# Optimization experiments

Hardware: AMD Instinct MI355X
Metric: run time of the kernel (lower is better)

The kernel has to match this reference:

```python
import jax, jax.numpy as jnp
import numpy as np

N_NODES = 20000
N_EDGES = 320000
L = 512   # input feature dim (size_dict['small'][0])
D = 256   # hidden dim (feat_channel), heads=1 so head_dim = 256
C = 2     # n_classes


def setup_inputs() -> dict:
    key = jax.random.key(0)
    ks = jax.random.split(key, 18)
    s = 0.02
    inp = {
        "x": jax.random.normal(ks[0], (N_NODES, L), jnp.float32),
        "edge_index": jax.random.randint(ks[1], (2, N_EDGES), 0, N_NODES, dtype=jnp.int32),
        "label": 1,
        # TransformerConv(L, D, heads=1): query/key/value + root skip projections
        "Wq": jax.random.normal(ks[2], (L, D), jnp.float32) * s,
        "bq": jax.random.normal(ks[3], (D,), jnp.float32) * s,
        "Wk": jax.random.normal(ks[4], (L, D), jnp.float32) * s,
        "bk": jax.random.normal(ks[5], (D,), jnp.float32) * s,
        "Wv": jax.random.normal(ks[6], (L, D), jnp.float32) * s,
        "bv": jax.random.normal(ks[7], (D,), jnp.float32) * s,
        "Ws": jax.random.normal(ks[8], (L, D), jnp.float32) * s,
        "bs": jax.random.normal(ks[9], (D,), jnp.float32) * s,
        # GlobalAdaptPooling: tanh-MLP attention (heads = n_classes) + per-class classifier
        "Wa1": jax.random.normal(ks[10], (D, D), jnp.float32) * s,
        "ba1": jax.random.normal(ks[11], (D,), jnp.float32) * s,
        "Wa2": jax.random.normal(ks[12], (D, C), jnp.float32) * s,
        "ba2": jax.random.normal(ks[13], (C,), jnp.float32) * s,
        "Wc": jax.random.normal(ks[14], (C, D), jnp.float32) * s,
        "bc": jax.random.normal(ks[15], (C,), jnp.float32) * s,
    }
    return inp


def _forward(x, edge_index, label, Wq, bq, Wk, bk, Wv, bv, Ws, bs, Wa1, ba1, Wa2, ba2, Wc, bc):
    n = x.shape[0]
    src = edge_index[0]  # message source j
    dst = edge_index[1]  # message target i
    # --- TransformerConv (heads=1, concat, root_weight=True) ---
    q = x @ Wq + bq                      # [N, D]
    k = x @ Wk + bk
    v = x @ Wv + bv
    score = jnp.sum(q[dst] * k[src], axis=-1) / jnp.sqrt(jnp.float32(D))  # [E]
    # segment softmax over incoming edges of each target node
    m = jax.ops.segment_max(score, dst, num_segments=n)
    e = jnp.exp(score - m[dst])
    den = jax.ops.segment_sum(e, dst, num_segments=n)
    alpha = e / den[dst]                 # [E]
    agg = jax.ops.segment_sum(alpha[:, None] * v[src], dst, num_segments=n)  # [N, D]
    h = agg + x @ Ws + bs
    # --- act: GELU (torch exact/erf) ---
    h = jax.nn.gelu(h, approximate=False)
    # --- GlobalAdaptPooling: node attention with n_classes heads ---
    scores = jnp.tanh(h @ Wa1 + ba1) @ Wa2 + ba2      # [N, C]
    attn = jax.nn.softmax(scores, axis=0)             # softmax over nodes
    M = attn.T @ h                                    # [C, D] per-class bag embedding
    logits = (jnp.sum(M * Wc, axis=1) + bc)[None, :]  # [1, C]
    Y_prob = jax.nn.softmax(logits, axis=1)
    A = attn[:, label]                                # [N] attention for target class
    return logits, Y_prob, A


def reference(x, edge_index, label, Wq, bq, Wk, bk, Wv, bv, Ws, bs, Wa1, ba1, Wa2, ba2, Wc, bc):
    return _forward(x, edge_index, label, Wq, bq, Wk, bk, Wv, bv, Ws, bs, Wa1, ba1, Wa2, ba2, Wc, bc)
```

## Files before the change

kernel.cpp:

```cpp
#include <hip/hip_runtime.h>
#include <hip/hip_bf16.h>
#include <math.h>

typedef float f32x4_t __attribute__((ext_vector_type(4)));
typedef float f32x2_t __attribute__((ext_vector_type(2)));
typedef __bf16 bf16x8_t __attribute__((ext_vector_type(8)));

__device__ __forceinline__ float bf2f(unsigned int u){
  union { float f; unsigned int i; } x; x.i = u << 16; return x.f;
}
__device__ __forceinline__ unsigned short f2bf(float f){
  unsigned int x = __float_as_uint(f);
  unsigned int r = (x + 0x7fffu + ((x >> 16) & 1u)) >> 16;
  return (unsigned short)r;
}
__device__ __forceinline__ unsigned int pk2bf(float a, float b){
  return (unsigned int)f2bf(a) | ((unsigned int)f2bf(b) << 16);
}
__device__ __forceinline__ int swz4(int r){ return (r ^ (r >> 2) ^ (r >> 4)) & 3; }

__device__ __forceinline__ void unp8s(uint4 w, float* f, float s){
  f[0] = bf2f(w.x & 0xffffu) * s; f[1] = bf2f(w.x >> 16) * s;
  f[2] = bf2f(w.y & 0xffffu) * s; f[3] = bf2f(w.y >> 16) * s;
  f[4] = bf2f(w.z & 0xffffu) * s; f[5] = bf2f(w.z >> 16) * s;
  f[6] = bf2f(w.w & 0xffffu) * s; f[7] = bf2f(w.w >> 16) * s;
}
__device__ __forceinline__ void unpf8(unsigned int w, float* f){
  f32x2_t lo = __builtin_amdgcn_cvt_pk_f32_fp8(w, false);
  f32x2_t hi = __builtin_amdgcn_cvt_pk_f32_fp8(w, true);
  f[0] = lo[0]; f[1] = lo[1]; f[2] = hi[0]; f[3] = hi[1];
}

#define GLOAD16(gsrc, ldst) \
  __builtin_amdgcn_global_load_lds((const __attribute__((address_space(1))) unsigned int*)(gsrc), \
                                   (__attribute__((address_space(3))) unsigned int*)(ldst), 16, 0, 0)

__global__ void zero_buf(uint4* __restrict__ p, int n16){
  int i = blockIdx.x * 256 + threadIdx.x;
  if (i < n16) p[i] = make_uint4(0, 0, 0, 0);
}

__global__ void prep(const float* __restrict__ x,
                     const float* __restrict__ Wq, const float* __restrict__ Wk,
                     const float* __restrict__ Wv, const float* __restrict__ Ws,
                     const float* __restrict__ bq, const float* __restrict__ bk,
                     const float* __restrict__ bv, const float* __restrict__ bs,
                     const float* __restrict__ Wa1, const int* __restrict__ ei,
                     unsigned short* __restrict__ xbf, unsigned short* __restrict__ wcatT,
                     float* __restrict__ bcat, unsigned short* __restrict__ wa1T,
                     int* __restrict__ deg, int n, int ne, int nbcv){
  const int b = blockIdx.x, tid = threadIdx.x;
  if (b < 2048){
    int idx = b * 256 + tid;
    int c = idx >> 9, k = idx & 511;
    int sel = c >> 8, cc = c & 255;
    const float* W = (sel == 0) ? Wq : (sel == 1) ? Wk : (sel == 2) ? Wv : Ws;
    int p = ((k >> 3) & 3) ^ swz4(c & 127);
    int dst = c * 512 + (k & ~31) + p * 8 + (k & 7);
    wcatT[dst] = f2bf(W[k * 256 + cc]);
    if (idx < 1024){
      int sel2 = idx >> 8, cc2 = idx & 255;
      const float* B = (sel2 == 0) ? bq : (sel2 == 1) ? bk : (sel2 == 2) ? bv : bs;
      bcat[idx] = B[cc2];
    }
  } else if (b < 2304){
    int idx = (b - 2048) * 256 + tid;
    int c = idx >> 8, k = idx & 255;
    wa1T[idx] = f2bf(Wa1[k * 256 + c]);
  } else if (b < 2304 + nbcv){
    int idx = (b - 2304) * 256 + tid;
    if (idx < n * 64){
      int node = idx >> 6, un = idx & 63;
      int k0 = (un >> 2) * 32, u = un & 3;
      const float* src = x + (size_t)node * 512 + k0 + u * 8;
      float4 f0 = *reinterpret_cast<const float4*>(src);
      float4 f1 = *reinterpret_cast<const float4*>(src + 4);
      uint4 o;
      o.x = pk2bf(f0.x, f0.y); o.y = pk2bf(f0.z, f0.w);
      o.z = pk2bf(f1.x, f1.y); o.w = pk2bf(f1.z, f1.w);
      int p = u ^ swz4(node & 127);
      *reinterpret_cast<uint4*>(xbf + (size_t)node * 512 + k0 + p * 8) = o;
    }
  } else {
    int i = (b - 2304 - nbcv) * 256 + tid;
    if (i < ne) atomicAdd(&deg[ei[ne + i]], 1);
  }
}

__global__ __launch_bounds__(256) void gemm_qkvs(const unsigned short* __restrict__ xbf,
                                                 const unsigned short* __restrict__ wcatT,
                                                 const float* __restrict__ bcat,
                                                 unsigned short* __restrict__ qbf,
                                                 unsigned short* __restrict__ sbf,
                                                 unsigned char* __restrict__ kv8,
                                                 int n_nodes, int mblocks){
  __shared__ __align__(16) unsigned char smem[49152];
  const int tid = threadIdx.x;
  const int lane = tid & 63, wave = tid >> 6;
  const int wm = wave >> 1, wn = wave & 1;
  const int g = (blockIdx.x & 7) * mblocks + (blockIdx.x >> 3);
  const int m_blk = g >> 3, n_blk = g & 7;
  const int m0 = m_blk * 128, n0 = n_blk * 128;
  const int lrow = lane >> 2;
  const int lcol = (lane & 3) * 8;
  const int rA0 = min(m0 + wave * 16 + lrow, n_nodes - 1);
  const int rA1 = min(m0 + (wave + 4) * 16 + lrow, n_nodes - 1);
  const int rB0 = n0 + wave * 16 + lrow;
  const int rB1 = rB0 + 64;
  const int r = lane & 15, q4 = lane >> 4;
  const unsigned short* aG0 = xbf   + (size_t)rA0 * 512 + lcol;
  const unsigned short* aG1 = xbf   + (size_t)rA1 * 512 + lcol;
  const unsigned short* bG0 = wcatT + (size_t)rB0 * 512 + lcol;
  const unsigned short* bG1 = wcatT + (size_t)rB1 * 512 + lcol;
  int aoff[4], boff[4];
  #pragma unroll
  for (int mi = 0; mi < 4; mi++){ int rr = wm * 64 + mi * 16 + r; aoff[mi] = rr * 32 + ((q4 ^ swz4(rr)) * 8); }
  #pragma unroll
  for (int ni = 0; ni < 4; ni++){ int rb = wn * 64 + ni * 16 + r; boff[ni] = rb * 32 + ((q4 ^ swz4(rb)) * 8); }
  f32x4_t acc[4][4] = {};
#define STAGE(base, k0) { \
    unsigned short* As_ = (unsigned short*)(smem + (base)); \
    unsigned short* Bs_ = (unsigned short*)(smem + (base) + 8192); \
    GLOAD16(aG0 + (k0), &As_[wave * 512]); \
    GLOAD16(aG1 + (k0), &As_[(wave + 4) * 512]); \
    GLOAD16(bG0 + (k0), &Bs_[wave * 512]); \
    GLOAD16(bG1 + (k0), &Bs_[(wave + 4) * 512]); \
  }
  STAGE(0, 0);
  STAGE(16384, 32);
  int cbase = 0;
  int sbase = 32768;
  for (int t = 0; t < 16; t++){
    if (t + 2 < 16){
      STAGE(sbase, (t + 2) * 32);
      asm volatile("s_waitcnt vmcnt(8)" ::: "memory");
    } else if (t + 1 < 16){
      asm volatile("s_waitcnt vmcnt(4)" ::: "memory");
    } else {
      asm volatile("s_waitcnt vmcnt(0)" ::: "memory");
    }
    __builtin_amdgcn_s_barrier();
    asm volatile("" ::: "memory");
    const unsigned short* As = (const unsigned short*)(smem + cbase);
    const unsigned short* Bs = (const unsigned short*)(smem + cbase + 8192);
    bf16x8_t a[4], b[4];
    #pragma unroll
    for (int mi = 0; mi < 4; mi++) a[mi] = *reinterpret_cast<const bf16x8_t*>(&As[aoff[mi]]);
    #pragma unroll
    for (int ni = 0; ni < 4; ni++) b[ni] = *reinterpret_cast<const bf16x8_t*>(&Bs[boff[ni]]);
    #pragma unroll
    for (int mi = 0; mi < 4; mi++)
      #pragma unroll
      for (int ni = 0; ni < 4; ni++)
        acc[mi][ni] = __builtin_amdgcn_mfma_f32_16x16x32_bf16(b[ni], a[mi], acc[mi][ni], 0, 0, 0);
    __builtin_amdgcn_s_barrier();
    asm volatile("" ::: "memory");
    cbase += 16384; if (cbase == 49152) cbase = 0;
    sbase += 16384; if (sbase == 49152) sbase = 0;
  }
#undef STAGE
  const bool isQ = (n_blk < 2), isS = (n_blk >= 6);
  if (isQ || isS){
    unsigned short* St = (unsigned short*)smem;
    unsigned short* outp = isQ ? qbf : sbf;
    const int colhalf = isQ ? n_blk : (n_blk - 6);
    #pragma unroll
    for (int ch = 0; ch < 2; ch++){
      if (wm == ch){
        #pragma unroll
        for (int mi = 0; mi < 4; mi++){
          #pragma unroll
          for (int ni = 0; ni < 4; ni++){
            int mloc = mi * 16 + r;
            int nl = wn * 64 + ni * 16 + q4 * 4;
            float4 bb = *reinterpret_cast<const float4*>(&bcat[n0 + nl]);
            uint2 w;
            w.x = pk2bf(acc[mi][ni][0] + bb.x, acc[mi][ni][1] + bb.y);
            w.y = pk2bf(acc[mi][ni][2] + bb.z, acc[mi][ni][3] + bb.w);
            *reinterpret_cast<uint2*>(&St[mloc * 152 + nl]) = w;
          }
        }
      }
      __syncthreads();
      #pragma unroll
      for (int it = 0; it < 4; it++){
        int u = it * 256 + tid;
        int row = u >> 4, seg = (u & 15) * 8;
        int node = m0 + ch * 64 + row;
        if (node < n_nodes){
          uint4 v = *reinterpret_cast<const uint4*>(&St[row * 152 + seg]);
          *reinterpret_cast<uint4*>(outp + (size_t)node * 256 + colhalf * 128 + seg) = v;
        }
      }
      __syncthreads();
    }
  } else {
    unsigned char* St8 = smem;
    #pragma unroll
    for (int ch = 0; ch < 2; ch++){
      if (wm == ch){
        #pragma unroll
        for (int mi = 0; mi < 4; mi++){
          #pragma unroll
          for (int ni = 0; ni < 4; ni++){
            int mloc = mi * 16 + r;
            int nl = wn * 64 + ni * 16 + q4 * 4;
            float4 bb = *reinterpret_cast<const float4*>(&bcat[n0 + nl]);
            int u = 0;
            u = __builtin_amdgcn_cvt_pk_fp8_f32(acc[mi][ni][0] + bb.x, acc[mi][ni][1] + bb.y, u, false);
            u = __builtin_amdgcn_cvt_pk_fp8_f32(acc[mi][ni][2] + bb.z, acc[mi][ni][3] + bb.w, u, true);
            *reinterpret_cast<unsigned int*>(&St8[mloc * 144 + nl]) = (unsigned int)u;
          }
        }
      }
      __syncthreads();
      #pragma unroll
      for (int it = 0; it < 2; it++){
        int u = it * 256 + tid;
        int row = u >> 3, seg = (u & 7) * 16;
        int node = m0 + ch * 64 + row;
        if (node < n_nodes){
          uint4 v = *reinterpret_cast<const uint4*>(&St8[row * 144 + seg]);
          *reinterpret_cast<uint4*>(kv8 + (size_t)node * 512 + (n_blk - 2) * 128 + seg) = v;
        }
      }
      __syncthreads();
    }
  }
}

__global__ void scan_deg(const int* __restrict__ deg, int* __restrict__ rowstart, int n, int ne){
  __shared__ int sm[1024];
  int tid = threadIdx.x;
  int per = (n + 1023) / 1024;
  int start = tid * per;
  int sum = 0;
  for (int i = 0; i < per; i++){
    int idx = start + i;
    sum += (idx < n) ? deg[idx] : 0;
  }
  sm[tid] = sum; __syncthreads();
  for (int off = 1; off < 1024; off <<= 1){
    int t = (tid >= off) ? sm[tid - off] : 0;
    __syncthreads();
    sm[tid] += t;
    __syncthreads();
  }
  int run = sm[tid] - sum;
  for (int i = 0; i < per; i++){
    int idx = start + i;
    if (idx < n){
      rowstart[idx] = run;
      run += deg[idx];
    }
  }
  if (tid == 0) rowstart[n] = ne;
}

__global__ void scatter_edges(const int* __restrict__ ei, const int* __restrict__ rowstart,
                              int* __restrict__ cursor, int* __restrict__ csrsrc, int ne){
  int i = blockIdx.x * 256 + threadIdx.x;
  if (i < ne){
    int d = ei[ne + i];
    int pos = atomicAdd(&cursor[d], 1);
    csrsrc[rowstart[d] + pos] = ei[i] << 9;
  }
}

__global__ __launch_bounds__(256) void edge_attn(const unsigned short* __restrict__ qbf,
                                                 const unsigned short* __restrict__ sbf,
                                                 const unsigned char* __restrict__ kv8,
                                                 const int* __restrict__ rowstart,
                                                 const int* __restrict__ csrsrc,
                                                 unsigned short* __restrict__ hbf, int n_nodes){
  const int tid = threadIdx.x;
  const int lane = tid & 63, wave = tid >> 6;
  const int g = lane >> 4, t = lane & 15;
  const int chain = g & 1;
  const int node = blockIdx.x * 8 + wave * 2 + (g >> 1);
  const bool active = node < n_nodes;
  const int nd = active ? node : 0;
  const float qs = 0.0625f * 1.44269504088896340736f;
  float q[16];
  {
    const unsigned short* qp = qbf + (size_t)nd * 256 + t * 16;
    uint4 w0 = *reinterpret_cast<const uint4*>(qp);
    uint4 w1 = *reinterpret_cast<const uint4*>(qp + 8);
    unp8s(w0, q, qs); unp8s(w1, q + 8, qs);
  }
  int rs = rowstart[nd];
  int re = active ? rowstart[nd + 1] : rs;
  float m = -1e30f, den = 0.f;
  float acc[16];
  #pragma unroll
  for (int j = 0; j < 16; j++) acc[j] = 0.f;
  const int i0 = rs + chain;
  uint4 kA = make_uint4(0,0,0,0), vA = kA, kB = kA, vB = kA;
  if (i0 < re){
    const unsigned char* p1 = kv8 + (size_t)csrsrc[i0] + t * 16;
    kA = *reinterpret_cast<const uint4*>(p1);
    vA = *reinterpret_cast<const uint4*>(p1 + 256);
    if (i0 + 2 < re){
      const unsigned char* p2 = kv8 + (size_t)csrsrc[i0 + 2] + t * 16;
      kB = *reinterpret_cast<const uint4*>(p2);
      vB = *reinterpret_cast<const uint4*>(p2 + 256);
    }
  }
  for (int i = i0; i < re; i += 4){
    uint4 k1 = kA, v1 = vA, k2 = kB, v2 = vB;
    const bool has2 = (i + 2 < re);
    if (i + 4 < re){
      const unsigned char* p1 = kv8 + (size_t)csrsrc[i + 4] + t * 16;
      kA = *reinterpret_cast<const uint4*>(p1);
      vA = *reinterpret_cast<const uint4*>(p1 + 256);
      if (i + 6 < re){
        const unsigned char* p2 = kv8 + (size_t)csrsrc[i + 6] + t * 16;
        kB = *reinterpret_cast<const uint4*>(p2);
        vB = *reinterpret_cast<const uint4*>(p2 + 256);
      }
    }
    float kf1[16], kf2[16];
    unpf8(k1.x, kf1); unpf8(k1.y, kf1 + 4); unpf8(k1.z, kf1 + 8); unpf8(k1.w, kf1 + 12);
    unpf8(k2.x, kf2); unpf8(k2.y, kf2 + 4); unpf8(k2.z, kf2 + 8); unpf8(k2.w, kf2 + 12);
    float s1 = 0.f, s2 = 0.f;
    #pragma unroll
    for (int j = 0; j < 16; j++){ s1 = fmaf(q[j], kf1[j], s1); s2 = fmaf(q[j], kf2[j], s2); }
    s1 += __shfl_xor(s1, 1); s2 += __shfl_xor(s2, 1);
    s1 += __shfl_xor(s1, 2); s2 += __shfl_xor(s2, 2);
    s1 += __shfl_xor(s1, 4); s2 += __shfl_xor(s2, 4);
    s1 += __shfl_xor(s1, 8); s2 += __shfl_xor(s2, 8);
    if (!has2) s2 = -1e30f;
    float vf1[16], vf2[16];
    unpf8(v1.x, vf1); unpf8(v1.y, vf1 + 4); unpf8(v1.z, vf1 + 8); unpf8(v1.w, vf1 + 12);
    unpf8(v2.x, vf2); unpf8(v2.y, vf2 + 4); unpf8(v2.z, vf2 + 8); unpf8(v2.w, vf2 + 12);
    float mn = fmaxf(m, fmaxf(s1, s2));
    float sc = exp2f(m - mn);
    float e1 = exp2f(s1 - mn);
    float e2 = exp2f(s2 - mn);
    den = den * sc + e1 + e2;
    #pragma unroll
    for (int j = 0; j < 16; j++)
      acc[j] = fmaf(acc[j], sc, fmaf(e1, vf1[j], e2 * vf2[j]));
    m = mn;
  }
  {
    float mo  = __shfl_xor(m, 16);
    float dno = __shfl_xor(den, 16);
    float mn  = fmaxf(m, mo);
    float a_  = exp2f(m - mn);
    float b_  = exp2f(mo - mn);
    den = den * a_ + dno * b_;
    #pragma unroll
    for (int j = 0; j < 16; j++){
      float oth = __shfl_xor(acc[j], 16);
      acc[j] = acc[j] * a_ + oth * b_;
    }
  }
  float inv = (den > 0.f) ? 1.f / den : 0.f;
  const unsigned short* sp = sbf + (size_t)nd * 256 + t * 16;
  uint4 s0 = *reinterpret_cast<const uint4*>(sp);
  uint4 s1v = *reinterpret_cast<const uint4*>(sp + 8);
  float sf[16]; unp8s(s0, sf, 1.0f); unp8s(s1v, sf + 8, 1.0f);
  const float inv_sqrt2 = 0.70710678118654752f;
  unsigned int o[8];
  #pragma unroll
  for (int j = 0; j < 8; j++){
    float h0 = acc[2 * j] * inv + sf[2 * j];
    float h1 = acc[2 * j + 1] * inv + sf[2 * j + 1];
    h0 = 0.5f * h0 * (1.f + erff(h0 * inv_sqrt2));
    h1 = 0.5f * h1 * (1.f + erff(h1 * inv_sqrt2));
    o[j] = (unsigned int)f2bf(h0) | ((unsigned int)f2bf(h1) << 16);
  }
  if (active && chain == 0){
    uint4* dst = reinterpret_cast<uint4*>(hbf + (size_t)node * 256 + t * 16);
    dst[0] = make_uint4(o[0], o[1], o[2], o[3]);
    dst[1] = make_uint4(o[4], o[5], o[6], o[7]);
  }
}

__global__ __launch_bounds__(256) void mlp_mfma(const unsigned short* __restrict__ hbf,
                                                const unsigned short* __restrict__ wa1T,
                                                const float* __restrict__ ba1,
                                                const float* __restrict__ Wa2,
                                                const float* __restrict__ ba2,
                                                float* __restrict__ s2, int n_nodes){
  __shared__ __align__(16) unsigned short As[64 * 72];
  __shared__ float s2s[64][2];
  const int tid = threadIdx.x;
  const int lane = tid & 63, wave = tid >> 6;
  const int m0 = blockIdx.x * 64;
  const int c0 = wave * 64;
  const int r = lane & 15, rg = (lane >> 4) * 4;
  if (tid < 128) s2s[tid >> 1][tid & 1] = 0.f;
  f32x4_t acc[4][4] = {};
  for (int k0 = 0; k0 < 256; k0 += 64){
    int arow = tid >> 2, akc = (tid & 3) * 16;
    uint4 a0v = make_uint4(0,0,0,0), a1v = make_uint4(0,0,0,0);
    if (m0 + arow < n_nodes){
      const unsigned short* src = hbf + (size_t)(m0 + arow) * 256 + k0 + akc;
      a0v = *reinterpret_cast<const uint4*>(src);
      a1v = *reinterpret_cast<const uint4*>(src + 8);
    }
    *reinterpret_cast<uint4*>(&As[arow * 72 + akc]) = a0v;
    *reinterpret_cast<uint4*>(&As[arow * 72 + akc + 8]) = a1v;
    __syncthreads();
    #pragma unroll
    for (int kk = 0; kk < 2; kk++){
      int kg = kk * 32 + (lane >> 4) * 8;
      bf16x8_t a[4], b[4];
      #pragma unroll
      for (int mi = 0; mi < 4; mi++)
        a[mi] = *reinterpret_cast<const bf16x8_t*>(&As[(mi * 16 + r) * 72 + kg]);
      #pragma unroll
      for (int ni = 0; ni < 4; ni++)
        b[ni] = *reinterpret_cast<const bf16x8_t*>(wa1T + (size_t)(c0 + ni * 16 + r) * 256 + k0 + kg);
      #pragma unroll
      for (int mi = 0; mi < 4; mi++)
        #pragma unroll
        for (int ni = 0; ni < 4; ni++)
          acc[mi][ni] = __builtin_amdgcn_mfma_f32_16x16x32_bf16(a[mi], b[ni], acc[mi][ni], 0, 0, 0);
    }
    __syncthreads();
  }
  float w20[4], w21[4], b1c[4];
  #pragma unroll
  for (int ni = 0; ni < 4; ni++){
    int col = c0 + ni * 16 + r;
    w20[ni] = Wa2[col * 2]; w21[ni] = Wa2[col * 2 + 1]; b1c[ni] = ba1[col];
  }
  #pragma unroll
  for (int mi = 0; mi < 4; mi++){
    #pragma unroll
    for (int j = 0; j < 4; j++){
      float t0 = 0.f, t1 = 0.f;
      #pragma unroll
      for (int ni = 0; ni < 4; ni++){
        float t = tanhf(acc[mi][ni][j] + b1c[ni]);
        t0 += t * w20[ni]; t1 += t * w21[ni];
      }
      t0 += __shfl_xor(t0, 1); t0 += __shfl_xor(t0, 2);
      t0 += __shfl_xor(t0, 4); t0 += __shfl_xor(t0, 8);
      t1 += __shfl_xor(t1, 1); t1 += __shfl_xor(t1, 2);
      t1 += __shfl_xor(t1, 4); t1 += __shfl_xor(t1, 8);
      if (r == 0){
        int row = mi * 16 + rg + j;
        atomicAdd(&s2s[row][0], t0);
        atomicAdd(&s2s[row][1], t1);
      }
    }
  }
  __syncthreads();
  if (tid < 128){
    int row = tid >> 1, c = tid & 1;
    int node = m0 + row;
    if (node < n_nodes) s2[node * 2 + c] = s2s[row][c] + ba2[c];
  }
}

__global__ void col_reduce(const float* __restrict__ s2, float* __restrict__ red, int n){
  __shared__ float sm[1024];
  __shared__ float mshare[2];
  int tid = threadIdx.x;
  float mx0 = -INFINITY, mx1 = -INFINITY;
  for (int i = tid; i < n; i += 1024){
    mx0 = fmaxf(mx0, s2[2 * i]);
    mx1 = fmaxf(mx1, s2[2 * i + 1]);
  }
  sm[tid] = mx0; __syncthreads();
  for (int off = 512; off > 0; off >>= 1){
    if (tid < off) sm[tid] = fmaxf(sm[tid], sm[tid + off]);
    __syncthreads();
  }
  if (tid == 0) mshare[0] = sm[0];
  __syncthreads();
  sm[tid] = mx1; __syncthreads();
  for (int off = 512; off > 0; off >>= 1){
    if (tid < off) sm[tid] = fmaxf(sm[tid], sm[tid + off]);
    __syncthreads();
  }
  if (tid == 0) mshare[1] = sm[0];
  __syncthreads();
  float m0 = mshare[0], m1 = mshare[1];
  float s0 = 0.f, s1 = 0.f;
  for (int i = tid; i < n; i += 1024){
    s0 += expf(s2[2 * i] - m0);
    s1 += expf(s2[2 * i + 1] - m1);
  }
  sm[tid] = s0; __syncthreads();
  for (int off = 512; off > 0; off >>= 1){
    if (tid < off) sm[tid] += sm[tid + off];
    __syncthreads();
  }
  float den0 = sm[0];
  __syncthreads();
  sm[tid] = s1; __syncthreads();
  for (int off = 512; off > 0; off >>= 1){
    if (tid < off) sm[tid] += sm[tid + off];
    __syncthreads();
  }
  if (tid == 0){
    red[0] = m0; red[1] = m1; red[2] = den0; red[3] = sm[0];
  }
}

__global__ __launch_bounds__(256) void attn_M(const float* __restrict__ s2, const float* __restrict__ red,
                                              const unsigned short* __restrict__ hbf, const int* __restrict__ label,
                                              float* __restrict__ Mbuf, float* __restrict__ outA, int n){
  __shared__ float a0s[256], a1s[256];
  int tid = threadIdx.x;
  int n0 = blockIdx.x * 256;
  int node = n0 + tid;
  float m0 = red[0], m1 = red[1];
  float i0 = 1.f / red[2], i1 = 1.f / red[3];
  float a0 = 0.f, a1 = 0.f;
  if (node < n){
    a0 = expf(s2[2 * node] - m0) * i0;
    a1 = expf(s2[2 * node + 1] - m1) * i1;
    outA[node] = (label[0] == 0) ? a0 : a1;
  }
  a0s[tid] = a0; a1s[tid] = a1;
  __syncthreads();
  int d = tid;
  float M0 = 0.f, M1 = 0.f;
  int cnt = min(256, n - n0);
  for (int i = 0; i < cnt; i++){
    float hv = bf2f((unsigned int)hbf[(size_t)(n0 + i) * 256 + d]);
    M0 += a0s[i] * hv;
    M1 += a1s[i] * hv;
  }
  atomicAdd(&Mbuf[d], M0);
  atomicAdd(&Mbuf[256 + d], M1);
}

__global__ void final_k(const float* __restrict__ Mbuf, const float* __restrict__ Wc,
                        const float* __restrict__ bc, float* __restrict__ out){
  __shared__ float sm[256];
  __shared__ float l0s;
  int tid = threadIdx.x;
  float p0 = Mbuf[tid] * Wc[tid];
  float p1 = Mbuf[256 + tid] * Wc[256 + tid];
  sm[tid] = p0; __syncthreads();
  for (int off = 128; off > 0; off >>= 1){
    if (tid < off) sm[tid] += sm[tid + off];
    __syncthreads();
  }
  if (tid == 0) l0s = sm[0];
  __syncthreads();
  sm[tid] = p1; __syncthreads();
  for (int off = 128; off > 0; off >>= 1){
    if (tid < off) sm[tid] += sm[tid + off];
    __syncthreads();
  }
  if (tid == 0){
    float l0 = l0s + bc[0];
    float l1 = sm[0] + bc[1];
    out[0] = l0; out[1] = l1;
    float mx = fmaxf(l0, l1);
    float e0 = expf(l0 - mx), e1 = expf(l1 - mx);
    float inv = 1.f / (e0 + e1);
    out[2] = e0 * inv; out[3] = e1 * inv;
  }
}

extern "C" void kernel_launch(void* const* d_in, const int* in_sizes, int n_in,
                              void* d_out, int out_size, void* d_ws, size_t ws_size,
                              hipStream_t stream) {
  const float* x   = (const float*)d_in[0];
  const int*   ei  = (const int*)d_in[1];
  const int*   lab = (const int*)d_in[2];
  const float* Wq  = (const float*)d_in[3];
  const float* bq  = (const float*)d_in[4];
  const float* Wk  = (const float*)d_in[5];
  const float* bk  = (const float*)d_in[6];
  const float* Wv  = (const float*)d_in[7];
  const float* bv  = (const float*)d_in[8];
  const float* Ws  = (const float*)d_in[9];
  const float* bs  = (const float*)d_in[10];
  const float* Wa1 = (const float*)d_in[11];
  const float* ba1 = (const float*)d_in[12];
  const float* Wa2 = (const float*)d_in[13];
  const float* ba2 = (const float*)d_in[14];
  const float* Wc  = (const float*)d_in[15];
  const float* bc  = (const float*)d_in[16];
  float* out = (float*)d_out;

  const int n  = in_sizes[0] / 512;
  const int ne = in_sizes[1] / 2;

  char* ws = (char*)d_ws;
  size_t off = 0;
  auto take = [&](size_t bytes){ size_t r = off; off += (bytes + 255) & ~(size_t)255; return r; };
  unsigned short* wcatT  = (unsigned short*)(ws + take((size_t)1024 * 512 * 2));
  float*          bcat   = (float*)(ws + take(1024 * 4));
  unsigned short* xbf    = (unsigned short*)(ws + take((size_t)n * 512 * 2));
  unsigned short* qbf    = (unsigned short*)(ws + take((size_t)n * 256 * 2));
  unsigned short* sbf    = (unsigned short*)(ws + take((size_t)n * 256 * 2));
  unsigned char*  kv8    = (unsigned char*)(ws + take((size_t)n * 512));
  unsigned short* hbf    = (unsigned short*)(ws + take((size_t)n * 256 * 2));
  unsigned short* wa1T   = (unsigned short*)(ws + take((size_t)256 * 256 * 2));
  float*          s2     = (float*)(ws + take((size_t)n * 2 * 4));
  size_t zoff = off;
  int*            deg    = (int*)(ws + take((size_t)n * 4));
  int*            cursor = (int*)(ws + take((size_t)n * 4));
  float*          Mbuf   = (float*)(ws + take(512 * 4));
  size_t zlen = off - zoff;
  int*            rowst  = (int*)(ws + take((size_t)(n + 1) * 4));
  int*            csrsrc = (int*)(ws + take((size_t)ne * 4));
  float*          red    = (float*)(ws + take(4 * 4));

  const int z16 = (int)(zlen / 16);
  zero_buf<<<(z16 + 255) / 256, 256, 0, stream>>>((uint4*)(ws + zoff), z16);

  const int nbcv = (n * 64 + 255) / 256;
  const int nbdh = (ne + 255) / 256;
  prep<<<2304 + nbcv + nbdh, 256, 0, stream>>>(x, Wq, Wk, Wv, Ws, bq, bk, bv, bs, Wa1, ei,
                                               xbf, wcatT, bcat, wa1T, deg, n, ne, nbcv);
  const int mblocks = (n + 127) / 128;
  gemm_qkvs<<<8 * mblocks, 256, 0, stream>>>(xbf, wcatT, bcat, qbf, sbf, kv8, n, mblocks);
  scan_deg<<<1, 1024, 0, stream>>>(deg, rowst, n, ne);
  scatter_edges<<<(ne + 255) / 256, 256, 0, stream>>>(ei, rowst, cursor, csrsrc, ne);
  edge_attn<<<(n + 7) / 8, 256, 0, stream>>>(qbf, sbf, kv8, rowst, csrsrc, hbf, n);
  mlp_mfma<<<(n + 63) / 64, 256, 0, stream>>>(hbf, wa1T, ba1, Wa2, ba2, s2, n);
  col_reduce<<<1, 1024, 0, stream>>>(s2, red, n);
  attn_M<<<(n + 255) / 256, 256, 0, stream>>>(s2, red, hbf, lab, Mbuf, out + 4, n);
  final_k<<<1, 256, 0, stream>>>(Mbuf, Wc, bc, out);
  (void)ws_size; (void)out_size; (void)n_in;
}
```

Before: 193.1 us.

## Load GEMM B fragments directly from global into registers; vectorize attention pooling

The QKVS GEMM stops staging the weight (B) tile through shared memory. Each wave now reads its B fragments straight from global memory into registers with a one-step register prefetch, while only the A tile is staged, through a 5-slot LDS ring that runs three steps ahead. This drops the second barrier per k-step and the weight swizzle, so the weight layout becomes plain row-major. Separately, attn_M switches to 16-byte vector loads of h, with 8 node lanes per block, and reduces through shared memory before the global atomics, replacing strided 2-byte loads. The risk is higher global/L2 traffic for B, since it is no longer shared across waves through LDS, and more register pressure.

```diff
diff --git a/kernel.cpp b/kernel.cpp
--- a/kernel.cpp
+++ b/kernel.cpp
@@ -55,9 +55,7 @@
     int c = idx >> 9, k = idx & 511;
     int sel = c >> 8, cc = c & 255;
     const float* W = (sel == 0) ? Wq : (sel == 1) ? Wk : (sel == 2) ? Wv : Ws;
-    int p = ((k >> 3) & 3) ^ swz4(c & 127);
-    int dst = c * 512 + (k & ~31) + p * 8 + (k & 7);
-    wcatT[dst] = f2bf(W[k * 256 + cc]);
+    wcatT[c * 512 + k] = f2bf(W[k * 256 + cc]);
     if (idx < 1024){
       int sel2 = idx >> 8, cc2 = idx & 255;
       const float* B = (sel2 == 0) ? bq : (sel2 == 1) ? bk : (sel2 == 2) ? bv : bs;
@@ -94,7 +92,7 @@
                                                  unsigned short* __restrict__ sbf,
                                                  unsigned char* __restrict__ kv8,
                                                  int n_nodes, int mblocks){
-  __shared__ __align__(16) unsigned char smem[49152];
+  __shared__ __align__(16) unsigned char smem[40960];
   const int tid = threadIdx.x;
   const int lane = tid & 63, wave = tid >> 6;
   const int wm = wave >> 1, wn = wave & 1;
@@ -105,60 +103,57 @@
   const int lcol = (lane & 3) * 8;
   const int rA0 = min(m0 + wave * 16 + lrow, n_nodes - 1);
   const int rA1 = min(m0 + (wave + 4) * 16 + lrow, n_nodes - 1);
-  const int rB0 = n0 + wave * 16 + lrow;
-  const int rB1 = rB0 + 64;
   const int r = lane & 15, q4 = lane >> 4;
-  const unsigned short* aG0 = xbf   + (size_t)rA0 * 512 + lcol;
-  const unsigned short* aG1 = xbf   + (size_t)rA1 * 512 + lcol;
-  const unsigned short* bG0 = wcatT + (size_t)rB0 * 512 + lcol;
-  const unsigned short* bG1 = wcatT + (size_t)rB1 * 512 + lcol;
-  int aoff[4], boff[4];
+  const unsigned short* aG0 = xbf + (size_t)rA0 * 512 + lcol;
+  const unsigned short* aG1 = xbf + (size_t)rA1 * 512 + lcol;
+  const unsigned short* bP  = wcatT + (size_t)(n0 + wn * 64 + r) * 512 + q4 * 8;
+  int aoff[4];
   #pragma unroll
   for (int mi = 0; mi < 4; mi++){ int rr = wm * 64 + mi * 16 + r; aoff[mi] = rr * 32 + ((q4 ^ swz4(rr)) * 8); }
+  f32x4_t acc[4][4] = {};
+#define STAGE_A(base, kk) { \
+    unsigned short* As_ = (unsigned short*)(smem + (base)); \
+    GLOAD16(aG0 + (kk), &As_[wave * 512]); \
+    GLOAD16(aG1 + (kk), &As_[(wave + 4) * 512]); \
+  }
+  STAGE_A(0, 0);
+  STAGE_A(8192, 32);
+  STAGE_A(16384, 64);
+  bf16x8_t bcur[4], bnext[4];
   #pragma unroll
-  for (int ni = 0; ni < 4; ni++){ int rb = wn * 64 + ni * 16 + r; boff[ni] = rb * 32 + ((q4 ^ swz4(rb)) * 8); }
-  f32x4_t acc[4][4] = {};
-#define STAGE(base, k0) { \
-    unsigned short* As_ = (unsigned short*)(smem + (base)); \
-    unsigned short* Bs_ = (unsigned short*)(smem + (base) + 8192); \
-    GLOAD16(aG0 + (k0), &As_[wave * 512]); \
-    GLOAD16(aG1 + (k0), &As_[(wave + 4) * 512]); \
-    GLOAD16(bG0 + (k0), &Bs_[wave * 512]); \
-    GLOAD16(bG1 + (k0), &Bs_[(wave + 4) * 512]); \
-  }
-  STAGE(0, 0);
-  STAGE(16384, 32);
+  for (int ni = 0; ni < 4; ni++)
+    bcur[ni] = *reinterpret_cast<const bf16x8_t*>(bP + ni * 8192);
   int cbase = 0;
-  int sbase = 32768;
+  int sbase = 24576;
   for (int t = 0; t < 16; t++){
-    if (t + 2 < 16){
-      STAGE(sbase, (t + 2) * 32);
-      asm volatile("s_waitcnt vmcnt(8)" ::: "memory");
-    } else if (t + 1 < 16){
-      asm volatile("s_waitcnt vmcnt(4)" ::: "memory");
-    } else {
-      asm volatile("s_waitcnt vmcnt(0)" ::: "memory");
-    }
+    asm volatile("s_waitcnt vmcnt(2)" ::: "memory");
     __builtin_amdgcn_s_barrier();
     asm volatile("" ::: "memory");
     const unsigned short* As = (const unsigned short*)(smem + cbase);
-    const unsigned short* Bs = (const unsigned short*)(smem + cbase + 8192);
-    bf16x8_t a[4], b[4];
+    bf16x8_t a[4];
     #pragma unroll
     for (int mi = 0; mi < 4; mi++) a[mi] = *reinterpret_cast<const bf16x8_t*>(&As[aoff[mi]]);
-    #pragma unroll
-    for (int ni = 0; ni < 4; ni++) b[ni] = *reinterpret_cast<const bf16x8_t*>(&Bs[boff[ni]]);
+    {
+      int kb = (t + 1 < 16 ? t + 1 : 15) * 32;
+      #pragma unroll
+      for (int ni = 0; ni < 4; ni++)
+        bnext[ni] = *reinterpret_cast<const bf16x8_t*>(bP + ni * 8192 + kb);
+      int ks = (t + 3 < 16 ? t + 3 : 15) * 32;
+      STAGE_A(sbase, ks);
+    }
     #pragma unroll
     for (int mi = 0; mi < 4; mi++)
       #pragma unroll
       for (int ni = 0; ni < 4; ni++)
-        acc[mi][ni] = __builtin_amdgcn_mfma_f32_16x16x32_bf16(b[ni], a[mi], acc[mi][ni], 0, 0, 0);
-    __builtin_amdgcn_s_barrier();
-    asm volatile("" ::: "memory");
-    cbase += 16384; if (cbase == 49152) cbase = 0;
-    sbase += 16384; if (sbase == 49152) sbase = 0;
-  }
-#undef STAGE
+        acc[mi][ni] = __builtin_amdgcn_mfma_f32_16x16x32_bf16(bcur[ni], a[mi], acc[mi][ni], 0, 0, 0);
+    #pragma unroll
+    for (int ni = 0; ni < 4; ni++) bcur[ni] = bnext[ni];
+    cbase += 8192; if (cbase == 40960) cbase = 0;
+    sbase += 8192; if (sbase == 40960) sbase = 0;
+  }
+#undef STAGE_A
+  asm volatile("s_waitcnt vmcnt(0)" ::: "memory");
+  __syncthreads();
   const bool isQ = (n_blk < 2), isS = (n_blk >= 6);
   if (isQ || isS){
     unsigned short* St = (unsigned short*)smem;
@@ -507,6 +502,7 @@
                                               const unsigned short* __restrict__ hbf, const int* __restrict__ label,
                                               float* __restrict__ Mbuf, float* __restrict__ outA, int n){
   __shared__ float a0s[256], a1s[256];
+  __shared__ float Ms[512];
   int tid = threadIdx.x;
   int n0 = blockIdx.x * 256;
   int node = n0 + tid;
@@ -519,17 +515,38 @@
     outA[node] = (label[0] == 0) ? a0 : a1;
   }
   a0s[tid] = a0; a1s[tid] = a1;
-  __syncthreads();
-  int d = tid;
-  float M0 = 0.f, M1 = 0.f;
-  int cnt = min(256, n - n0);
-  for (int i = 0; i < cnt; i++){
-    float hv = bf2f((unsigned int)hbf[(size_t)(n0 + i) * 256 + d]);
-    M0 += a0s[i] * hv;
-    M1 += a1s[i] * hv;
-  }
-  atomicAdd(&Mbuf[d], M0);
-  atomicAdd(&Mbuf[256 + d], M1);
+  Ms[tid] = 0.f; Ms[tid + 256] = 0.f;
+  __syncthreads();
+  const int dgrp = tid & 31;
+  const int nl = tid >> 5;
+  float M0[8] = {}, M1[8] = {};
+  for (int i = nl; i < 256; i += 8){
+    int nd = n0 + i;
+    if (nd >= n) break;
+    uint4 w = *reinterpret_cast<const uint4*>(hbf + (size_t)nd * 256 + dgrp * 8);
+    float f[8]; unp8s(w, f, 1.0f);
+    float A0 = a0s[i], A1 = a1s[i];
+    #pragma unroll
+    for (int j = 0; j < 8; j++){
+      M0[j] = fmaf(A0, f[j], M0[j]);
+      M1[j] = fmaf(A1, f[j], M1[j]);
+    }
+  }
+  #pragma unroll
+  for (int j = 0; j < 8; j++){
+    M0[j] += __shfl_xor(M0[j], 32);
+    M1[j] += __shfl_xor(M1[j], 32);
+  }
+  if ((tid & 32) == 0){
+    #pragma unroll
+    for (int j = 0; j < 8; j++){
+      atomicAdd(&Ms[dgrp * 8 + j], M0[j]);
+      atomicAdd(&Ms[256 + dgrp * 8 + j], M1[j]);
+    }
+  }
+  __syncthreads();
+  atomicAdd(&Mbuf[tid], Ms[tid]);
+  atomicAdd(&Mbuf[256 + tid], Ms[tid + 256]);
 }
 
 __global__ void final_k(const float* __restrict__ Mbuf, const float* __restrict__ Wc,
```

Result: slower. 223.4 us (+15.7%).

## Use four edge chains per node in edge_attn and vectorize attn_M reduction

Applied to the files above, without the earlier changes.

edge_attn now assigns one wave per node, with four 16-lane groups each walking every fourth edge pair, instead of two chains per node and two nodes per wave. The partial softmax states are merged with a two-step shuffle butterfly. This is meant to shorten the per-node serial edge chain and expose more memory-level parallelism, at the cost of twice as many blocks and idle lanes on low-degree nodes. attn_M switches from scalar strided bf16 loads to 16-byte vector loads across 8 node lanes, followed by a shared-memory atomic reduction, to cut load instructions.

```diff
diff --git a/kernel.cpp b/kernel.cpp
--- a/kernel.cpp
+++ b/kernel.cpp
@@ -276,8 +276,8 @@
   const int tid = threadIdx.x;
   const int lane = tid & 63, wave = tid >> 6;
   const int g = lane >> 4, t = lane & 15;
-  const int chain = g & 1;
-  const int node = blockIdx.x * 8 + wave * 2 + (g >> 1);
+  const int chain = g;
+  const int node = blockIdx.x * 4 + wave;
   const bool active = node < n_nodes;
   const int nd = active ? node : 0;
   const float qs = 0.0625f * 1.44269504088896340736f;
@@ -300,21 +300,21 @@
     const unsigned char* p1 = kv8 + (size_t)csrsrc[i0] + t * 16;
     kA = *reinterpret_cast<const uint4*>(p1);
     vA = *reinterpret_cast<const uint4*>(p1 + 256);
-    if (i0 + 2 < re){
-      const unsigned char* p2 = kv8 + (size_t)csrsrc[i0 + 2] + t * 16;
+    if (i0 + 4 < re){
+      const unsigned char* p2 = kv8 + (size_t)csrsrc[i0 + 4] + t * 16;
       kB = *reinterpret_cast<const uint4*>(p2);
       vB = *reinterpret_cast<const uint4*>(p2 + 256);
     }
   }
-  for (int i = i0; i < re; i += 4){
+  for (int i = i0; i < re; i += 8){
     uint4 k1 = kA, v1 = vA, k2 = kB, v2 = vB;
-    const bool has2 = (i + 2 < re);
-    if (i + 4 < re){
-      const unsigned char* p1 = kv8 + (size_t)csrsrc[i + 4] + t * 16;
+    const bool has2 = (i + 4 < re);
+    if (i + 8 < re){
+      const unsigned char* p1 = kv8 + (size_t)csrsrc[i + 8] + t * 16;
       kA = *reinterpret_cast<const uint4*>(p1);
       vA = *reinterpret_cast<const uint4*>(p1 + 256);
-      if (i + 6 < re){
-        const unsigned char* p2 = kv8 + (size_t)csrsrc[i + 6] + t * 16;
+      if (i + 12 < re){
+        const unsigned char* p2 = kv8 + (size_t)csrsrc[i + 12] + t * 16;
         kB = *reinterpret_cast<const uint4*>(p2);
         vB = *reinterpret_cast<const uint4*>(p2 + 256);
       }
@@ -343,18 +343,20 @@
       acc[j] = fmaf(acc[j], sc, fmaf(e1, vf1[j], e2 * vf2[j]));
     m = mn;
   }
-  {
-    float mo  = __shfl_xor(m, 16);
-    float dno = __shfl_xor(den, 16);
+  #pragma unroll
+  for (int step = 16; step <= 32; step <<= 1){
+    float mo  = __shfl_xor(m, step);
+    float dno = __shfl_xor(den, step);
     float mn  = fmaxf(m, mo);
     float a_  = exp2f(m - mn);
     float b_  = exp2f(mo - mn);
     den = den * a_ + dno * b_;
     #pragma unroll
     for (int j = 0; j < 16; j++){
-      float oth = __shfl_xor(acc[j], 16);
+      float oth = __shfl_xor(acc[j], step);
       acc[j] = acc[j] * a_ + oth * b_;
     }
+    m = mn;
   }
   float inv = (den > 0.f) ? 1.f / den : 0.f;
   const unsigned short* sp = sbf + (size_t)nd * 256 + t * 16;
@@ -371,7 +373,7 @@
     h1 = 0.5f * h1 * (1.f + erff(h1 * inv_sqrt2));
     o[j] = (unsigned int)f2bf(h0) | ((unsigned int)f2bf(h1) << 16);
   }
-  if (active && chain == 0){
+  if (active && g == 0){
     uint4* dst = reinterpret_cast<uint4*>(hbf + (size_t)node * 256 + t * 16);
     dst[0] = make_uint4(o[0], o[1], o[2], o[3]);
     dst[1] = make_uint4(o[4], o[5], o[6], o[7]);
@@ -507,6 +509,7 @@
                                               const unsigned short* __restrict__ hbf, const int* __restrict__ label,
                                               float* __restrict__ Mbuf, float* __restrict__ outA, int n){
   __shared__ float a0s[256], a1s[256];
+  __shared__ float Ms[512];
   int tid = threadIdx.x;
   int n0 = blockIdx.x * 256;
   int node = n0 + tid;
@@ -519,17 +522,38 @@
     outA[node] = (label[0] == 0) ? a0 : a1;
   }
   a0s[tid] = a0; a1s[tid] = a1;
+  Ms[tid] = 0.f; Ms[tid + 256] = 0.f;
   __syncthreads();
-  int d = tid;
-  float M0 = 0.f, M1 = 0.f;
-  int cnt = min(256, n - n0);
-  for (int i = 0; i < cnt; i++){
-    float hv = bf2f((unsigned int)hbf[(size_t)(n0 + i) * 256 + d]);
-    M0 += a0s[i] * hv;
-    M1 += a1s[i] * hv;
-  }
-  atomicAdd(&Mbuf[d], M0);
-  atomicAdd(&Mbuf[256 + d], M1);
+  const int dgrp = tid & 31;
+  const int nl = tid >> 5;
+  float M0[8] = {}, M1[8] = {};
+  for (int i = nl; i < 256; i += 8){
+    int nd = n0 + i;
+    if (nd >= n) break;
+    uint4 w = *reinterpret_cast<const uint4*>(hbf + (size_t)nd * 256 + dgrp * 8);
+    float f[8]; unp8s(w, f, 1.0f);
+    float A0 = a0s[i], A1 = a1s[i];
+    #pragma unroll
+    for (int j = 0; j < 8; j++){
+      M0[j] = fmaf(A0, f[j], M0[j]);
+      M1[j] = fmaf(A1, f[j], M1[j]);
+    }
+  }
+  #pragma unroll
+  for (int j = 0; j < 8; j++){
+    M0[j] += __shfl_xor(M0[j], 32);
+    M1[j] += __shfl_xor(M1[j], 32);
+  }
+  if ((tid & 32) == 0){
+    #pragma unroll
+    for (int j = 0; j < 8; j++){
+      atomicAdd(&Ms[dgrp * 8 + j], M0[j]);
+      atomicAdd(&Ms[256 + dgrp * 8 + j], M1[j]);
+    }
+  }
+  __syncthreads();
+  atomicAdd(&Mbuf[tid], Ms[tid]);
+  atomicAdd(&Mbuf[256 + tid], Ms[tid + 256]);
 }
 
 __global__ void final_k(const float* __restrict__ Mbuf, const float* __restrict__ Wc,
@@ -619,7 +643,7 @@
   gemm_qkvs<<<8 * mblocks, 256, 0, stream>>>(xbf, wcatT, bcat, qbf, sbf, kv8, n, mblocks);
   scan_deg<<<1, 1024, 0, stream>>>(deg, rowst, n, ne);
   scatter_edges<<<(ne + 255) / 256, 256, 0, stream>>>(ei, rowst, cursor, csrsrc, ne);
-  edge_attn<<<(n + 7) / 8, 256, 0, stream>>>(qbf, sbf, kv8, rowst, csrsrc, hbf, n);
+  edge_attn<<<(n + 3) / 4, 256, 0, stream>>>(qbf, sbf, kv8, rowst, csrsrc, hbf, n);
   mlp_mfma<<<(n + 63) / 64, 256, 0, stream>>>(hbf, wa1T, ba1, Wa2, ba2, s2, n);
   col_reduce<<<1, 1024, 0, stream>>>(s2, red, n);
   attn_M<<<(n + 255) / 256, 256, 0, stream>>>(s2, red, hbf, lab, Mbuf, out + 4, n);
```

After: 200.2 us. 1.04x slower.
